# Optimization experiments

Hardware: AMD Instinct MI355X
Metric: run time of the kernel (lower is better)

Reference implementation:

```python
import jax, jax.numpy as jnp
import numpy as np

T, B, FEAT, HID, NCLS = 256, 64, 256, 1024, 257


def hamilton_block(W):
    # W: [4, di, do] components (r,i,j,k) -> full real block matrix [4*di, 4*do]
    Wr, Wi, Wj, Wk = W[0], W[1], W[2], W[3]
    row0 = jnp.concatenate([Wr, Wi, Wj, Wk], axis=-1)
    row1 = jnp.concatenate([-Wi, Wr, -Wk, Wj], axis=-1)
    row2 = jnp.concatenate([-Wj, Wk, Wr, -Wi], axis=-1)
    row3 = jnp.concatenate([-Wk, -Wj, Wi, Wr], axis=-1)
    return jnp.concatenate([row0, row1, row2, row3], axis=-2)


def setup_inputs() -> dict:
    key = jax.random.key(0)
    ks = jax.random.split(key, 7)
    x = jax.random.normal(ks[0], (T, B, FEAT), dtype=jnp.float32)
    sx = 1.0 / np.sqrt(FEAT)
    sh = 1.0 / np.sqrt(HID)
    # 4 gates (f,i,o,c) x 4 quaternion components x [feat/4, hid/4]
    Wx = jax.random.normal(ks[1], (4, 4, FEAT // 4, HID // 4), dtype=jnp.float32) * sx
    bx = jax.random.normal(ks[2], (4, HID), dtype=jnp.float32) * sx
    Wh = jax.random.normal(ks[3], (4, 4, HID // 4, HID // 4), dtype=jnp.float32) * sh
    Wo = jax.random.normal(ks[4], (HID, NCLS), dtype=jnp.float32) * sh
    bo = jax.random.normal(ks[5], (NCLS,), dtype=jnp.float32) * sh
    return {"x": x, "Wx": Wx, "bx": bx, "Wh": Wh, "Wo": Wo, "bo": bo}


def reference(x, Wx, bx, Wh, Wo, bo):
    # Build full real Hamilton-product matrices per gate.
    Wx_full = jax.vmap(hamilton_block)(Wx)  # [4, FEAT, HID]
    Wh_full = jax.vmap(hamilton_block)(Wh)  # [4, HID, HID]
    # Precompute input-to-hidden gate terms for all timesteps: [4, T, B, HID]
    gx = jnp.einsum('tbf,gfh->gtbh', x, Wx_full) + bx[:, None, None, :]

    def step(carry, gx_t):  # gx_t: [4, B, HID]
        h, c = carry
        gh = jnp.einsum('bh,gho->gbo', h, Wh_full)  # [4, B, HID]
        ft = jax.nn.sigmoid(gx_t[0] + gh[0])
        it = jax.nn.sigmoid(gx_t[1] + gh[1])
        ot = jax.nn.sigmoid(gx_t[2] + gh[2])
        at = gx_t[3] + gh[3]
        c = it * jnp.tanh(at) + ft * c
        h = ot * jnp.tanh(c)
        return (h, c), h

    h0 = jnp.zeros((B, HID), dtype=x.dtype)
    _, hs = jax.lax.scan(step, (h0, h0), jnp.moveaxis(gx, 1, 0))  # hs: [T, B, HID]
    return jnp.einsum('tbh,hc->tbc', hs, Wo) + bo  # [T, B, NCLS]
```

## Files before the change

kernel.cpp:

```cpp
#include <hip/hip_runtime.h>
#include <hip/hip_bf16.h>
#include <math.h>

#define T 256
#define B 64
#define FEAT 256
#define HID 1024
#define NCLS 257
#define KSTEPS 40
#define BH (B * HID)
#define BFEAT (B * FEAT)
#define NBLK 128
#define NTHR 512

typedef __attribute__((ext_vector_type(8))) short short8v;
typedef __attribute__((ext_vector_type(4))) float floatx4;

__device__ __constant__ int   d_comp[4][4] = {{0,1,2,3},{1,0,3,2},{2,3,0,1},{3,2,1,0}};
__device__ __constant__ float d_sign[4][4] = {{ 1.f, 1.f, 1.f, 1.f},
                                              {-1.f, 1.f,-1.f, 1.f},
                                              {-1.f, 1.f, 1.f,-1.f},
                                              {-1.f,-1.f, 1.f, 1.f}};

__device__ __forceinline__ ushort f2bf(float f) {
    union { float f; unsigned u; } v; v.f = f;
    unsigned r = v.u + 0x7FFF + ((v.u >> 16) & 1);
    return (ushort)(r >> 16);
}

__device__ __forceinline__ float sigm(float v) { return 1.f / (1.f + __expf(-v)); }
__device__ __forceinline__ float tanh_fast(float v) { return 1.f - 2.f / (1.f + __expf(2.f * v)); }

__global__ __launch_bounds__(256) void conv_xpanel(const float* __restrict__ x,
                                                   ushort* __restrict__ xp) {
    int i = blockIdx.x * 256 + threadIdx.x;
    int k4 = i & 63, b = (i >> 6) & 63, t = i >> 12;
    int k = k4 * 4;
    float4 v = ((const float4*)x)[i];
    ushort4 o;
    o.x = f2bf(v.x); o.y = f2bf(v.y); o.z = f2bf(v.z); o.w = f2bf(v.w);
    *(ushort4*)(xp + (size_t)t * BFEAT + (k >> 3) * 512 + b * 8 + (k & 4)) = o;
}

__global__ __launch_bounds__(256) void prep_wcf(const float* __restrict__ Wh,
                                                const float* __restrict__ Wx,
                                                ushort* __restrict__ wcf) {
    int e = blockIdx.x * 256 + threadIdx.x;
    int j    = e & 7;
    int lane = (e >> 3) & 63;
    int r    = e >> 9;
    int ks   = r % 40;
    int s    = r / 40;
    int mt   = s & 1;
    int blk  = s >> 1;
    int c  = mt * 16 + (lane & 15);
    int hl = c >> 2, g = c & 3;
    int n  = blk * 8 + hl;
    int qq = n >> 8, bc = n & 255;
    int k  = ks * 32 + ((lane >> 4) << 3) + j;
    float v;
    if (k < HID) {
        int p = k >> 8, a = k & 255;
        v = d_sign[p][qq] * Wh[((g * 4 + d_comp[p][qq]) * 256 + a) * 256 + bc];
    } else {
        int kk = k - HID;
        int p = kk >> 6, a = kk & 63;
        v = d_sign[p][qq] * Wx[((g * 4 + d_comp[p][qq]) * 64 + a) * 256 + bc];
    }
    wcf[e] = f2bf(v);
}

__global__ __launch_bounds__(256) void prep_wof(const float* __restrict__ Wo,
                                                ushort* __restrict__ wof) {
    int e = blockIdx.x * 256 + threadIdx.x;
    int j    = e & 7;
    int lane = (e >> 3) & 63;
    int ks   = (e >> 9) & 31;
    int tile = e >> 14;
    int n = tile * 16 + (lane & 15);
    int k = ks * 32 + ((lane >> 4) << 3) + j;
    wof[e] = (n < NCLS) ? f2bf(Wo[k * NCLS + n]) : (ushort)0;
}

__global__ __launch_bounds__(256) void init_hc(ushort* __restrict__ hs0,
                                               uint* __restrict__ flags) {
    int i = blockIdx.x * 256 + threadIdx.x;
    hs0[i] = 0;
    if (i < NBLK) flags[i] = 0;
}

__global__ __launch_bounds__(512, 2) void qlstm_persist(
    const ushort* __restrict__ xp,
    const ushort* __restrict__ wcf,
    const float*  __restrict__ bx,
    ushort*       __restrict__ hsteps,
    uint*         __restrict__ flags)
{
    __shared__ float pre[2][64][36];

    const int tid   = threadIdx.x;
    const int blk   = blockIdx.x;
    const int w     = tid >> 6;
    const int lane  = tid & 63;
    const int khalf = w >> 2;
    const int bt    = w & 3;
    const int hofs  = khalf * 16;
    const int xofs  = khalf * 4;

    const short8v* wsrc = (const short8v*)wcf + (size_t)blk * 2 * KSTEPS * 64 + lane;
    short8v Ah[2][16], Ax[2][4];
    #pragma unroll
    for (int mt = 0; mt < 2; ++mt) {
        #pragma unroll
        for (int i = 0; i < 16; ++i) Ah[mt][i] = wsrc[(mt * KSTEPS + hofs + i) * 64];
        #pragma unroll
        for (int u = 0; u < 4; ++u)  Ax[mt][u] = wsrc[(mt * KSTEPS + 32 + xofs + u) * 64];
    }
    #pragma unroll
    for (int mt = 0; mt < 2; ++mt) {
        #pragma unroll
        for (int i = 0; i < 16; ++i) asm volatile("" : "+v"(Ah[mt][i]));
        #pragma unroll
        for (int u = 0; u < 4; ++u)  asm volatile("" : "+v"(Ax[mt][u]));
    }

    const int gb = tid >> 3;
    const int hc = tid & 7;
    const int gn = blk * 8 + hc;
    const float bxf = bx[gn], bxi = bx[HID + gn];
    const float bxo = bx[2 * HID + gn], bxa = bx[3 * HID + gn];
    float c_reg = 0.f;

    const int boff = (lane >> 4) * 512 + (bt * 16 + (lane & 15)) * 8;

    for (int t = 0; t < T; ++t) {
        floatx4 acc0 = {0.f,0.f,0.f,0.f}, acc1 = {0.f,0.f,0.f,0.f};

        const ushort* xrow = xp + (size_t)t * BFEAT + boff;
        #pragma unroll
        for (int u = 0; u < 4; ++u) {
            short8v bv = *(const short8v*)(xrow + (xofs + u) * 2048);
            acc0 = __builtin_amdgcn_mfma_f32_16x16x32_bf16(Ax[0][u], bv, acc0, 0, 0, 0);
            acc1 = __builtin_amdgcn_mfma_f32_16x16x32_bf16(Ax[1][u], bv, acc1, 0, 0, 0);
        }

        if (t > 0) {
            const uint tgt = (uint)t;
            for (;;) {
                uint f0 = __hip_atomic_load(flags + lane,      __ATOMIC_RELAXED, __HIP_MEMORY_SCOPE_AGENT);
                uint f1 = __hip_atomic_load(flags + 64 + lane, __ATOMIC_RELAXED, __HIP_MEMORY_SCOPE_AGENT);
                if (__all((f0 >= tgt) && (f1 >= tgt))) break;
                __builtin_amdgcn_s_sleep(1);
            }
        }

        const ushort* hrow = hsteps + (size_t)t * BH + boff;
        #pragma unroll
        for (int i = 0; i < 16; ++i) {
            short8v bv = *(const short8v*)(hrow + (hofs + i) * 2048);
            acc0 = __builtin_amdgcn_mfma_f32_16x16x32_bf16(Ah[0][i], bv, acc0, 0, 0, 0);
            acc1 = __builtin_amdgcn_mfma_f32_16x16x32_bf16(Ah[1][i], bv, acc1, 0, 0, 0);
        }

        {
            const int pb = bt * 16 + (lane & 15);
            const int pm = (lane >> 4) * 4;
            #pragma unroll
            for (int jj = 0; jj < 4; ++jj) {
                pre[khalf][pb][pm + jj]      = acc0[jj];
                pre[khalf][pb][16 + pm + jj] = acc1[jj];
            }
        }
        __syncthreads();

        {
            float4 p0 = *(const float4*)&pre[0][gb][hc * 4];
            float4 p1 = *(const float4*)&pre[1][gb][hc * 4];
            float f  = sigm(p0.x + p1.x + bxf);
            float i_ = sigm(p0.y + p1.y + bxi);
            float o  = sigm(p0.z + p1.z + bxo);
            float a  = p0.w + p1.w + bxa;
            c_reg = i_ * tanh_fast(a) + f * c_reg;
            float h = o * tanh_fast(c_reg);
            uint hvu = f2bf(h);
            ushort* hp = hsteps + (size_t)(t + 1) * BH + blk * 512 + tid;
            asm volatile("global_store_short %0, %1, off sc0 sc1"
                         :: "v"(hp), "v"(hvu) : "memory");
            asm volatile("s_waitcnt vmcnt(0)" ::: "memory");
        }
        __syncthreads();

        if (t < T - 1 && tid == 0)
            __hip_atomic_store(flags + blk, (uint)(t + 1),
                               __ATOMIC_RELAXED, __HIP_MEMORY_SCOPE_AGENT);
    }
}

__global__ __launch_bounds__(256) void outproj(const ushort* __restrict__ hsteps,
                                               const ushort* __restrict__ wof,
                                               const float* __restrict__ bo,
                                               float* __restrict__ out) {
    const int tt   = blockIdx.x;
    const int nt   = blockIdx.y;
    const int tid  = threadIdx.x;
    const int w    = tid >> 6;
    const int lane = tid & 63;
    const int b    = w * 16 + (lane & 15);
    const ushort* abase = hsteps + (size_t)(tt + 1) * BH + (lane >> 4) * 512 + b * 8;
    const short8v* wb  = (const short8v*)wof;

    floatx4 ac[4] = {{0.f,0.f,0.f,0.f},{0.f,0.f,0.f,0.f},
                     {0.f,0.f,0.f,0.f},{0.f,0.f,0.f,0.f}};
    #pragma unroll 4
    for (int ks = 0; ks < 32; ++ks) {
        short8v av = *(const short8v*)(abase + ks * 2048);
        #pragma unroll
        for (int ct = 0; ct < 4; ++ct)
            ac[ct] = __builtin_amdgcn_mfma_f32_16x16x32_bf16(
                av, wb[((nt * 4 + ct) * 32 + ks) * 64 + lane], ac[ct], 0, 0, 0);
    }
    const int orow = tt * 64 + w * 16 + (lane >> 4) * 4;
    #pragma unroll
    for (int ct = 0; ct < 4; ++ct) {
        int n = nt * 64 + ct * 16 + (lane & 15);
        if (n < NCLS) {
            float bias = bo[n];
            #pragma unroll
            for (int j = 0; j < 4; ++j)
                out[(size_t)(orow + j) * NCLS + n] = ac[ct][j] + bias;
        }
    }
}

extern "C" void kernel_launch(void* const* d_in, const int* in_sizes, int n_in,
                              void* d_out, int out_size, void* d_ws, size_t ws_size,
                              hipStream_t stream) {
    const float* x  = (const float*)d_in[0];
    const float* Wx = (const float*)d_in[1];
    const float* bx = (const float*)d_in[2];
    const float* Wh = (const float*)d_in[3];
    const float* Wo = (const float*)d_in[4];
    const float* bo = (const float*)d_in[5];
    float* out = (float*)d_out;

    ushort* xp     = (ushort*)d_ws;
    ushort* wcf    = xp  + (size_t)T * BFEAT;
    ushort* wof    = wcf + (size_t)NBLK * 2 * KSTEPS * 512;
    ushort* hsteps = wof + 327680;
    uint*   flags  = (uint*)(hsteps + (size_t)(T + 1) * BH);

    conv_xpanel<<<(T * B * FEAT / 4) / 256, 256, 0, stream>>>(x, xp);
    prep_wcf<<<(NBLK * 2 * KSTEPS * 512) / 256, 256, 0, stream>>>(Wh, Wx, wcf);
    prep_wof<<<(20 * 32 * 512) / 256, 256, 0, stream>>>(Wo, wof);
    init_hc<<<BH / 256, 256, 0, stream>>>(hsteps, flags);

    void* args[] = {(void*)&xp, (void*)&wcf, (void*)&bx, (void*)&hsteps, (void*)&flags};
    hipLaunchCooperativeKernel((void*)qlstm_persist, dim3(NBLK), dim3(NTHR),
                               args, 0, stream);

    outproj<<<dim3(T, 5), 256, 0, stream>>>(hsteps, wof, bo, out);
}
```

Baseline: 1.101 ms.

## Split batch into four independent groups to pipeline the recurrent LSTM steps

The persistent recurrence kernel is restructured so the batch of 64 is split into four 16-row groups, each with its own h panel slot and flag array. Phases interleave the groups, so a block computes group g while other groups' hidden states are still being published. The new version uses 256 blocks of 256 threads, each owning 4 hidden units with a 4-way K split, and software-prefetches the next x/h panels and flag values. The aim is to hide cross-block synchronization latency behind independent work. The cost is more phases, more flag traffic and smaller MFMA work per barrier.

```diff
diff --git a/kernel.cpp b/kernel.cpp
--- a/kernel.cpp
+++ b/kernel.cpp
@@ -7,11 +7,11 @@
 #define FEAT 256
 #define HID 1024
 #define NCLS 257
-#define KSTEPS 40
-#define BH (B * HID)
-#define BFEAT (B * FEAT)
-#define NBLK 128
-#define NTHR 512
+#define NBLK 256
+#define NTHR 256
+#define NPH (T * 4)
+#define HSLOT 16384
+#define XSLOT 4096
 
 typedef __attribute__((ext_vector_type(8))) short short8v;
 typedef __attribute__((ext_vector_type(4))) float floatx4;
@@ -36,10 +36,11 @@
     int i = blockIdx.x * 256 + threadIdx.x;
     int k4 = i & 63, b = (i >> 6) & 63, t = i >> 12;
     int k = k4 * 4;
+    int g = b >> 4, b16 = b & 15;
     float4 v = ((const float4*)x)[i];
     ushort4 o;
     o.x = f2bf(v.x); o.y = f2bf(v.y); o.z = f2bf(v.z); o.w = f2bf(v.w);
-    *(ushort4*)(xp + (size_t)t * BFEAT + (k >> 3) * 512 + b * 8 + (k & 4)) = o;
+    *(ushort4*)(xp + (size_t)(t * 4 + g) * XSLOT + (k >> 3) * 128 + b16 * 8 + (k & 7)) = o;
 }
 
 __global__ __launch_bounds__(256) void prep_wcf(const float* __restrict__ Wh,
@@ -50,22 +51,20 @@
     int lane = (e >> 3) & 63;
     int r    = e >> 9;
     int ks   = r % 40;
-    int s    = r / 40;
-    int mt   = s & 1;
-    int blk  = s >> 1;
-    int c  = mt * 16 + (lane & 15);
-    int hl = c >> 2, g = c & 3;
-    int n  = blk * 8 + hl;
+    int blk  = r / 40;
+    int c  = lane & 15;
+    int hl = c >> 2, gg = c & 3;
+    int n  = blk * 4 + hl;
     int qq = n >> 8, bc = n & 255;
     int k  = ks * 32 + ((lane >> 4) << 3) + j;
     float v;
     if (k < HID) {
         int p = k >> 8, a = k & 255;
-        v = d_sign[p][qq] * Wh[((g * 4 + d_comp[p][qq]) * 256 + a) * 256 + bc];
+        v = d_sign[p][qq] * Wh[((gg * 4 + d_comp[p][qq]) * 256 + a) * 256 + bc];
     } else {
         int kk = k - HID;
         int p = kk >> 6, a = kk & 63;
-        v = d_sign[p][qq] * Wx[((g * 4 + d_comp[p][qq]) * 64 + a) * 256 + bc];
+        v = d_sign[p][qq] * Wx[((gg * 4 + d_comp[p][qq]) * 64 + a) * 256 + bc];
     }
     wcf[e] = f2bf(v);
 }
@@ -82,144 +81,167 @@
     wof[e] = (n < NCLS) ? f2bf(Wo[k * NCLS + n]) : (ushort)0;
 }
 
-__global__ __launch_bounds__(256) void init_hc(ushort* __restrict__ hs0,
-                                               uint* __restrict__ flags) {
-    int i = blockIdx.x * 256 + threadIdx.x;
-    hs0[i] = 0;
-    if (i < NBLK) flags[i] = 0;
-}
-
-__global__ __launch_bounds__(512, 2) void qlstm_persist(
+__global__ __launch_bounds__(256) void init_flags(uint* __restrict__ flg) {
+    int i = threadIdx.x;
+    flg[i] = 0; flg[256 + i] = 0; flg[512 + i] = 0; flg[768 + i] = 0;
+}
+
+__global__ __launch_bounds__(256) void qlstm_persist(
     const ushort* __restrict__ xp,
     const ushort* __restrict__ wcf,
     const float*  __restrict__ bx,
-    ushort*       __restrict__ hsteps,
-    uint*         __restrict__ flags)
+    ushort*       __restrict__ hpan,
+    uint*         __restrict__ flg)
 {
-    __shared__ float pre[2][64][36];
-
-    const int tid   = threadIdx.x;
-    const int blk   = blockIdx.x;
-    const int w     = tid >> 6;
-    const int lane  = tid & 63;
-    const int khalf = w >> 2;
-    const int bt    = w & 3;
-    const int hofs  = khalf * 16;
-    const int xofs  = khalf * 4;
-
-    const short8v* wsrc = (const short8v*)wcf + (size_t)blk * 2 * KSTEPS * 64 + lane;
-    short8v Ah[2][16], Ax[2][4];
-    #pragma unroll
-    for (int mt = 0; mt < 2; ++mt) {
-        #pragma unroll
-        for (int i = 0; i < 16; ++i) Ah[mt][i] = wsrc[(mt * KSTEPS + hofs + i) * 64];
-        #pragma unroll
-        for (int u = 0; u < 4; ++u)  Ax[mt][u] = wsrc[(mt * KSTEPS + 32 + xofs + u) * 64];
-    }
-    #pragma unroll
-    for (int mt = 0; mt < 2; ++mt) {
-        #pragma unroll
-        for (int i = 0; i < 16; ++i) asm volatile("" : "+v"(Ah[mt][i]));
-        #pragma unroll
-        for (int u = 0; u < 4; ++u)  asm volatile("" : "+v"(Ax[mt][u]));
-    }
-
-    const int gb = tid >> 3;
-    const int hc = tid & 7;
-    const int gn = blk * 8 + hc;
+    __shared__ float pre[2][4][16][20];
+
+    const int tid  = threadIdx.x;
+    const int blk  = blockIdx.x;
+    const int kq   = tid >> 6;
+    const int lane = tid & 63;
+    const int ld_off = (lane >> 4) * 128 + (lane & 15) * 8;
+
+    const short8v* wsrc = (const short8v*)wcf + (size_t)blk * 40 * 64 + lane;
+    short8v Ah[8], Axr[2];
+    #pragma unroll
+    for (int i = 0; i < 8; ++i) Ah[i] = wsrc[(kq * 8 + i) * 64];
+    #pragma unroll
+    for (int u = 0; u < 2; ++u) Axr[u] = wsrc[(32 + kq * 2 + u) * 64];
+    #pragma unroll
+    for (int i = 0; i < 8; ++i) asm volatile("" : "+v"(Ah[i]));
+    #pragma unroll
+    for (int u = 0; u < 2; ++u) asm volatile("" : "+v"(Axr[u]));
+
+    const int gb_loc = lane >> 2;
+    const int ghc    = lane & 3;
+    const int gn     = blk * 4 + ghc;
     const float bxf = bx[gn], bxi = bx[HID + gn];
     const float bxo = bx[2 * HID + gn], bxa = bx[3 * HID + gn];
+    const int st_off = (blk >> 1) * 128 + gb_loc * 8 + (blk & 1) * 4 + ghc;
     float c_reg = 0.f;
 
-    const int boff = (lane >> 4) * 512 + (bt * 16 + (lane & 15)) * 8;
+    short8v hb[8], xv[2];
+    uint4 fcarry = make_uint4(~0u, ~0u, ~0u, ~0u);
+    {
+        const ushort* xs = xp;
+        #pragma unroll
+        for (int u = 0; u < 2; ++u)
+            xv[u] = *(const short8v*)(xs + (kq * 2 + u) * 512 + ld_off);
+    }
 
     for (int t = 0; t < T; ++t) {
-        floatx4 acc0 = {0.f,0.f,0.f,0.f}, acc1 = {0.f,0.f,0.f,0.f};
-
-        const ushort* xrow = xp + (size_t)t * BFEAT + boff;
         #pragma unroll
-        for (int u = 0; u < 4; ++u) {
-            short8v bv = *(const short8v*)(xrow + (xofs + u) * 2048);
-            acc0 = __builtin_amdgcn_mfma_f32_16x16x32_bf16(Ax[0][u], bv, acc0, 0, 0, 0);
-            acc1 = __builtin_amdgcn_mfma_f32_16x16x32_bf16(Ax[1][u], bv, acc1, 0, 0, 0);
+        for (int g = 0; g < 4; ++g) {
+            const int p = t * 4 + g;
+
+            floatx4 acc = {0.f, 0.f, 0.f, 0.f};
+            acc = __builtin_amdgcn_mfma_f32_16x16x32_bf16(Axr[0], xv[0], acc, 0, 0, 0);
+            acc = __builtin_amdgcn_mfma_f32_16x16x32_bf16(Axr[1], xv[1], acc, 0, 0, 0);
+            if (t > 0) {
+                #pragma unroll
+                for (int i = 0; i < 8; ++i)
+                    acc = __builtin_amdgcn_mfma_f32_16x16x32_bf16(Ah[i], hb[i], acc, 0, 0, 0);
+            }
+
+            const int p1 = p + 1;
+            if (p1 < NPH) {
+                const ushort* xs = xp + (size_t)p1 * XSLOT;
+                #pragma unroll
+                for (int u = 0; u < 2; ++u)
+                    xv[u] = *(const short8v*)(xs + (kq * 2 + u) * 512 + ld_off);
+            }
+
+            if (p1 < NPH && p1 >= 4) {
+                const uint tgt = (uint)(p1 >> 2);
+                const int g2 = p1 & 3;
+                uint4 fu = fcarry;
+                bool ok = fu.x >= tgt && fu.y >= tgt && fu.z >= tgt && fu.w >= tgt;
+                while (!__all(ok)) {
+                    __builtin_amdgcn_s_sleep(1);
+                    fu.x = __hip_atomic_load(flg + g2 * NBLK + lane,       __ATOMIC_RELAXED, __HIP_MEMORY_SCOPE_AGENT);
+                    fu.y = __hip_atomic_load(flg + g2 * NBLK + 64 + lane,  __ATOMIC_RELAXED, __HIP_MEMORY_SCOPE_AGENT);
+                    fu.z = __hip_atomic_load(flg + g2 * NBLK + 128 + lane, __ATOMIC_RELAXED, __HIP_MEMORY_SCOPE_AGENT);
+                    fu.w = __hip_atomic_load(flg + g2 * NBLK + 192 + lane, __ATOMIC_RELAXED, __HIP_MEMORY_SCOPE_AGENT);
+                    ok = fu.x >= tgt && fu.y >= tgt && fu.z >= tgt && fu.w >= tgt;
+                }
+                __builtin_amdgcn_sched_barrier(0);
+                const ushort* hs = hpan + (size_t)p1 * HSLOT;
+                #pragma unroll
+                for (int i = 0; i < 8; ++i)
+                    hb[i] = *(const short8v*)(hs + (kq * 8 + i) * 512 + ld_off);
+            }
+
+            {
+                const int p2 = p + 2;
+                if (p2 < NPH && p2 >= 4) {
+                    const int g3 = p2 & 3;
+                    fcarry.x = __hip_atomic_load(flg + g3 * NBLK + lane,       __ATOMIC_RELAXED, __HIP_MEMORY_SCOPE_AGENT);
+                    fcarry.y = __hip_atomic_load(flg + g3 * NBLK + 64 + lane,  __ATOMIC_RELAXED, __HIP_MEMORY_SCOPE_AGENT);
+                    fcarry.z = __hip_atomic_load(flg + g3 * NBLK + 128 + lane, __ATOMIC_RELAXED, __HIP_MEMORY_SCOPE_AGENT);
+                    fcarry.w = __hip_atomic_load(flg + g3 * NBLK + 192 + lane, __ATOMIC_RELAXED, __HIP_MEMORY_SCOPE_AGENT);
+                } else {
+                    fcarry = make_uint4(~0u, ~0u, ~0u, ~0u);
+                }
+            }
+
+            {
+                const int pb = lane & 15;
+                const int pm = (lane >> 4) * 4;
+                #pragma unroll
+                for (int jj = 0; jj < 4; ++jj)
+                    pre[g & 1][kq][pb][pm + jj] = acc[jj];
+            }
+            __syncthreads();
+
+            if (kq == g) {
+                float4 s0 = *(const float4*)&pre[g & 1][0][gb_loc][ghc * 4];
+                float4 s1 = *(const float4*)&pre[g & 1][1][gb_loc][ghc * 4];
+                float4 s2 = *(const float4*)&pre[g & 1][2][gb_loc][ghc * 4];
+                float4 s3 = *(const float4*)&pre[g & 1][3][gb_loc][ghc * 4];
+                float pf = s0.x + s1.x + s2.x + s3.x + bxf;
+                float pi = s0.y + s1.y + s2.y + s3.y + bxi;
+                float po = s0.z + s1.z + s2.z + s3.z + bxo;
+                float pa = s0.w + s1.w + s2.w + s3.w + bxa;
+                float f  = sigm(pf), i_ = sigm(pi), o = sigm(po);
+                c_reg = i_ * tanh_fast(pa) + f * c_reg;
+                float h = o * tanh_fast(c_reg);
+                uint hvu = f2bf(h);
+                ushort* hp = hpan + (size_t)(p + 4) * HSLOT + st_off;
+                asm volatile("global_store_short %0, %1, off sc0 sc1"
+                             :: "v"(hp), "v"(hvu) : "memory");
+                asm volatile("s_waitcnt vmcnt(0)" ::: "memory");
+                if (lane == 0)
+                    __hip_atomic_store(flg + g * NBLK + blk, (uint)(t + 1),
+                                       __ATOMIC_RELAXED, __HIP_MEMORY_SCOPE_AGENT);
+            }
         }
-
-        if (t > 0) {
-            const uint tgt = (uint)t;
-            for (;;) {
-                uint f0 = __hip_atomic_load(flags + lane,      __ATOMIC_RELAXED, __HIP_MEMORY_SCOPE_AGENT);
-                uint f1 = __hip_atomic_load(flags + 64 + lane, __ATOMIC_RELAXED, __HIP_MEMORY_SCOPE_AGENT);
-                if (__all((f0 >= tgt) && (f1 >= tgt))) break;
-                __builtin_amdgcn_s_sleep(1);
-            }
-        }
-
-        const ushort* hrow = hsteps + (size_t)t * BH + boff;
-        #pragma unroll
-        for (int i = 0; i < 16; ++i) {
-            short8v bv = *(const short8v*)(hrow + (hofs + i) * 2048);
-            acc0 = __builtin_amdgcn_mfma_f32_16x16x32_bf16(Ah[0][i], bv, acc0, 0, 0, 0);
-            acc1 = __builtin_amdgcn_mfma_f32_16x16x32_bf16(Ah[1][i], bv, acc1, 0, 0, 0);
-        }
-
-        {
-            const int pb = bt * 16 + (lane & 15);
-            const int pm = (lane >> 4) * 4;
-            #pragma unroll
-            for (int jj = 0; jj < 4; ++jj) {
-                pre[khalf][pb][pm + jj]      = acc0[jj];
-                pre[khalf][pb][16 + pm + jj] = acc1[jj];
-            }
-        }
-        __syncthreads();
-
-        {
-            float4 p0 = *(const float4*)&pre[0][gb][hc * 4];
-            float4 p1 = *(const float4*)&pre[1][gb][hc * 4];
-            float f  = sigm(p0.x + p1.x + bxf);
-            float i_ = sigm(p0.y + p1.y + bxi);
-            float o  = sigm(p0.z + p1.z + bxo);
-            float a  = p0.w + p1.w + bxa;
-            c_reg = i_ * tanh_fast(a) + f * c_reg;
-            float h = o * tanh_fast(c_reg);
-            uint hvu = f2bf(h);
-            ushort* hp = hsteps + (size_t)(t + 1) * BH + blk * 512 + tid;
-            asm volatile("global_store_short %0, %1, off sc0 sc1"
-                         :: "v"(hp), "v"(hvu) : "memory");
-            asm volatile("s_waitcnt vmcnt(0)" ::: "memory");
-        }
-        __syncthreads();
-
-        if (t < T - 1 && tid == 0)
-            __hip_atomic_store(flags + blk, (uint)(t + 1),
-                               __ATOMIC_RELAXED, __HIP_MEMORY_SCOPE_AGENT);
-    }
-}
-
-__global__ __launch_bounds__(256) void outproj(const ushort* __restrict__ hsteps,
+    }
+}
+
+__global__ __launch_bounds__(256) void outproj(const ushort* __restrict__ hpan,
                                                const ushort* __restrict__ wof,
                                                const float* __restrict__ bo,
                                                float* __restrict__ out) {
     const int tt   = blockIdx.x;
     const int nt   = blockIdx.y;
     const int tid  = threadIdx.x;
-    const int w    = tid >> 6;
+    const int g    = tid >> 6;
     const int lane = tid & 63;
-    const int b    = w * 16 + (lane & 15);
-    const ushort* abase = hsteps + (size_t)(tt + 1) * BH + (lane >> 4) * 512 + b * 8;
-    const short8v* wb  = (const short8v*)wof;
+    const ushort* abase = hpan + ((size_t)(tt + 1) * 4 + g) * HSLOT
+                          + (lane >> 4) * 128 + (lane & 15) * 8;
+    const short8v* wb = (const short8v*)wof;
 
     floatx4 ac[4] = {{0.f,0.f,0.f,0.f},{0.f,0.f,0.f,0.f},
                      {0.f,0.f,0.f,0.f},{0.f,0.f,0.f,0.f}};
     #pragma unroll 4
     for (int ks = 0; ks < 32; ++ks) {
-        short8v av = *(const short8v*)(abase + ks * 2048);
+        short8v av = *(const short8v*)(abase + ks * 512);
         #pragma unroll
         for (int ct = 0; ct < 4; ++ct)
             ac[ct] = __builtin_amdgcn_mfma_f32_16x16x32_bf16(
                 av, wb[((nt * 4 + ct) * 32 + ks) * 64 + lane], ac[ct], 0, 0, 0);
     }
-    const int orow = tt * 64 + w * 16 + (lane >> 4) * 4;
+    const int orow = tt * 64 + g * 16 + (lane >> 4) * 4;
     #pragma unroll
     for (int ct = 0; ct < 4; ++ct) {
         int n = nt * 64 + ct * 16 + (lane & 15);
@@ -243,20 +265,20 @@
     const float* bo = (const float*)d_in[5];
     float* out = (float*)d_out;
 
-    ushort* xp     = (ushort*)d_ws;
-    ushort* wcf    = xp  + (size_t)T * BFEAT;
-    ushort* wof    = wcf + (size_t)NBLK * 2 * KSTEPS * 512;
-    ushort* hsteps = wof + 327680;
-    uint*   flags  = (uint*)(hsteps + (size_t)(T + 1) * BH);
+    ushort* xp   = (ushort*)d_ws;
+    ushort* wcf  = xp  + (size_t)NPH * XSLOT;
+    ushort* wof  = wcf + (size_t)256 * 40 * 512;
+    ushort* hpan = wof + 327680;
+    uint*   flg  = (uint*)(hpan + (size_t)(NPH + 4) * HSLOT);
 
     conv_xpanel<<<(T * B * FEAT / 4) / 256, 256, 0, stream>>>(x, xp);
-    prep_wcf<<<(NBLK * 2 * KSTEPS * 512) / 256, 256, 0, stream>>>(Wh, Wx, wcf);
+    prep_wcf<<<(256 * 40 * 512) / 256, 256, 0, stream>>>(Wh, Wx, wcf);
     prep_wof<<<(20 * 32 * 512) / 256, 256, 0, stream>>>(Wo, wof);
-    init_hc<<<BH / 256, 256, 0, stream>>>(hsteps, flags);
-
-    void* args[] = {(void*)&xp, (void*)&wcf, (void*)&bx, (void*)&hsteps, (void*)&flags};
+    init_flags<<<1, 256, 0, stream>>>(flg);
+
+    void* args[] = {(void*)&xp, (void*)&wcf, (void*)&bx, (void*)&hpan, (void*)&flg};
     hipLaunchCooperativeKernel((void*)qlstm_persist, dim3(NBLK), dim3(NTHR),
                                args, 0, stream);
 
-    outproj<<<dim3(T, 5), 256, 0, stream>>>(hsteps, wof, bo, out);
-}
+    outproj<<<dim3(T, 5), 256, 0, stream>>>(hpan, wof, bo, out);
+}
```

Result: slower. 1.502 ms (+36.4%).

## Split persistent LSTM across batch chunks with per-chunk flags and panel layout

Applied to the files above, without the earlier changes.

The recurrent kernel now uses 256 blocks, each owning 16 hidden units for one 16-row batch chunk. Blocks synchronize only with the 64 blocks sharing their batch chunk rather than all blocks. The h and x panels are re-laid out per chunk so each block loads a contiguous 16-batch slab. Loads are batched through inline asm before the MFMAs, and half the threads sit idle in the gate stage. This is meant to shorten the per-step barrier and the per-block work, at the cost of more blocks, each weight tile being held by four blocks, and no overlap between the h loads and the MFMAs.

```diff
diff --git a/kernel.cpp b/kernel.cpp
--- a/kernel.cpp
+++ b/kernel.cpp
@@ -7,11 +7,12 @@
 #define FEAT 256
 #define HID 1024
 #define NCLS 257
-#define KSTEPS 40
-#define BH (B * HID)
-#define BFEAT (B * FEAT)
-#define NBLK 128
+#define NCH 4
+#define NCG 64
+#define NBLK 256
 #define NTHR 512
+#define HSLOT 16384
+#define XSLOT 4096
 
 typedef __attribute__((ext_vector_type(8))) short short8v;
 typedef __attribute__((ext_vector_type(4))) float floatx4;
@@ -36,10 +37,11 @@
     int i = blockIdx.x * 256 + threadIdx.x;
     int k4 = i & 63, b = (i >> 6) & 63, t = i >> 12;
     int k = k4 * 4;
+    int c = b >> 4, b16 = b & 15;
     float4 v = ((const float4*)x)[i];
     ushort4 o;
     o.x = f2bf(v.x); o.y = f2bf(v.y); o.z = f2bf(v.z); o.w = f2bf(v.w);
-    *(ushort4*)(xp + (size_t)t * BFEAT + (k >> 3) * 512 + b * 8 + (k & 4)) = o;
+    *(ushort4*)(xp + (size_t)(t * 4 + c) * XSLOT + (k >> 3) * 128 + b16 * 8 + (k & 7)) = o;
 }
 
 __global__ __launch_bounds__(256) void prep_wcf(const float* __restrict__ Wh,
@@ -51,11 +53,11 @@
     int r    = e >> 9;
     int ks   = r % 40;
     int s    = r / 40;
-    int mt   = s & 1;
-    int blk  = s >> 1;
+    int mt   = s & 3;
+    int cg   = s >> 2;
     int c  = mt * 16 + (lane & 15);
     int hl = c >> 2, g = c & 3;
-    int n  = blk * 8 + hl;
+    int n  = cg * 16 + hl;
     int qq = n >> 8, bc = n & 255;
     int k  = ks * 32 + ((lane >> 4) << 3) + j;
     float v;
@@ -82,100 +84,113 @@
     wof[e] = (n < NCLS) ? f2bf(Wo[k * NCLS + n]) : (ushort)0;
 }
 
-__global__ __launch_bounds__(256) void init_hc(ushort* __restrict__ hs0,
-                                               uint* __restrict__ flags) {
+__global__ __launch_bounds__(256) void init_hf(ushort* __restrict__ hpan,
+                                               uint* __restrict__ flg) {
     int i = blockIdx.x * 256 + threadIdx.x;
-    hs0[i] = 0;
-    if (i < NBLK) flags[i] = 0;
+    ((ushort4*)hpan)[i] = make_ushort4(0, 0, 0, 0);
+    if (blockIdx.x == 0) flg[threadIdx.x] = 0;
 }
 
 __global__ __launch_bounds__(512, 2) void qlstm_persist(
     const ushort* __restrict__ xp,
     const ushort* __restrict__ wcf,
     const float*  __restrict__ bx,
-    ushort*       __restrict__ hsteps,
-    uint*         __restrict__ flags)
+    ushort*       __restrict__ hpan,
+    uint*         __restrict__ flg)
 {
-    __shared__ float pre[2][64][36];
-
-    const int tid   = threadIdx.x;
-    const int blk   = blockIdx.x;
-    const int w     = tid >> 6;
-    const int lane  = tid & 63;
-    const int khalf = w >> 2;
-    const int bt    = w & 3;
-    const int hofs  = khalf * 16;
-    const int xofs  = khalf * 4;
-
-    const short8v* wsrc = (const short8v*)wcf + (size_t)blk * 2 * KSTEPS * 64 + lane;
-    short8v Ah[2][16], Ax[2][4];
+    __shared__ float pre[2][16][72];
+
+    const int tid  = threadIdx.x;
+    const int blk  = blockIdx.x;
+    const int ch   = blk & 3;
+    const int cg   = blk >> 2;
+    const int w    = tid >> 6;
+    const int lane = tid & 63;
+    const int mt   = w & 3;
+    const int kh   = w >> 2;
+    const int ld_off = (lane >> 4) * 128 + (lane & 15) * 8;
+
+    const ushort* wbase = wcf + ((size_t)(cg * 4 + mt) * 40 + kh * 20) * 512 + lane * 8;
+    short8v A[20];
     #pragma unroll
-    for (int mt = 0; mt < 2; ++mt) {
+    for (int i = 0; i < 20; ++i) {
+        const ushort* ap = wbase + i * 512;
+        asm volatile("global_load_dwordx4 %0, %1, off" : "=v"(A[i]) : "v"(ap));
+    }
+    asm volatile("s_waitcnt vmcnt(0)" ::: "memory");
+    __builtin_amdgcn_sched_barrier(0);
+
+    const int gb = tid >> 4;
+    const int hl = tid & 15;
+    const int gn = cg * 16 + hl;
+    float bxf = 0.f, bxi = 0.f, bxo = 0.f, bxa = 0.f;
+    if (tid < 256) {
+        bxf = bx[gn]; bxi = bx[HID + gn];
+        bxo = bx[2 * HID + gn]; bxa = bx[3 * HID + gn];
+    }
+    float c_reg = 0.f;
+    const int st_off = (cg * 2 + (hl >> 3)) * 128 + gb * 8 + (hl & 7);
+    uint* myflags = flg + ch * 64;
+
+    for (int t = 0; t < T; ++t) {
+        const ushort* hs = hpan + (size_t)(t * NCH + ch) * HSLOT;
+        const ushort* xs = xp   + (size_t)(t * NCH + ch) * XSLOT;
+
+        short8v Bf[20];
+        if (kh == 1) {
+            #pragma unroll
+            for (int i = 12; i < 20; ++i) {
+                const ushort* p = xs + (i - 12) * 512 + ld_off;
+                asm volatile("global_load_dwordx4 %0, %1, off" : "=v"(Bf[i]) : "v"(p));
+            }
+        }
+
+        if (t > 0) {
+            if (w == 0) {
+                const uint tgt = (uint)t;
+                for (;;) {
+                    uint f = __hip_atomic_load(myflags + lane, __ATOMIC_RELAXED,
+                                               __HIP_MEMORY_SCOPE_AGENT);
+                    if (__all(f >= tgt)) break;
+                    __builtin_amdgcn_s_sleep(1);
+                }
+            }
+            __syncthreads();
+        }
+
+        if (kh == 0) {
+            #pragma unroll
+            for (int i = 0; i < 20; ++i) {
+                const ushort* p = hs + i * 512 + ld_off;
+                asm volatile("global_load_dwordx4 %0, %1, off" : "=v"(Bf[i]) : "v"(p));
+            }
+        } else {
+            #pragma unroll
+            for (int i = 0; i < 12; ++i) {
+                const ushort* p = hs + (20 + i) * 512 + ld_off;
+                asm volatile("global_load_dwordx4 %0, %1, off" : "=v"(Bf[i]) : "v"(p));
+            }
+        }
+        asm volatile("s_waitcnt vmcnt(0)" ::: "memory");
+        __builtin_amdgcn_sched_barrier(0);
+
+        floatx4 a0 = {0.f,0.f,0.f,0.f}, a1 = {0.f,0.f,0.f,0.f};
         #pragma unroll
-        for (int i = 0; i < 16; ++i) Ah[mt][i] = wsrc[(mt * KSTEPS + hofs + i) * 64];
-        #pragma unroll
-        for (int u = 0; u < 4; ++u)  Ax[mt][u] = wsrc[(mt * KSTEPS + 32 + xofs + u) * 64];
-    }
-    #pragma unroll
-    for (int mt = 0; mt < 2; ++mt) {
-        #pragma unroll
-        for (int i = 0; i < 16; ++i) asm volatile("" : "+v"(Ah[mt][i]));
-        #pragma unroll
-        for (int u = 0; u < 4; ++u)  asm volatile("" : "+v"(Ax[mt][u]));
-    }
-
-    const int gb = tid >> 3;
-    const int hc = tid & 7;
-    const int gn = blk * 8 + hc;
-    const float bxf = bx[gn], bxi = bx[HID + gn];
-    const float bxo = bx[2 * HID + gn], bxa = bx[3 * HID + gn];
-    float c_reg = 0.f;
-
-    const int boff = (lane >> 4) * 512 + (bt * 16 + (lane & 15)) * 8;
-
-    for (int t = 0; t < T; ++t) {
-        floatx4 acc0 = {0.f,0.f,0.f,0.f}, acc1 = {0.f,0.f,0.f,0.f};
-
-        const ushort* xrow = xp + (size_t)t * BFEAT + boff;
-        #pragma unroll
-        for (int u = 0; u < 4; ++u) {
-            short8v bv = *(const short8v*)(xrow + (xofs + u) * 2048);
-            acc0 = __builtin_amdgcn_mfma_f32_16x16x32_bf16(Ax[0][u], bv, acc0, 0, 0, 0);
-            acc1 = __builtin_amdgcn_mfma_f32_16x16x32_bf16(Ax[1][u], bv, acc1, 0, 0, 0);
-        }
-
-        if (t > 0) {
-            const uint tgt = (uint)t;
-            for (;;) {
-                uint f0 = __hip_atomic_load(flags + lane,      __ATOMIC_RELAXED, __HIP_MEMORY_SCOPE_AGENT);
-                uint f1 = __hip_atomic_load(flags + 64 + lane, __ATOMIC_RELAXED, __HIP_MEMORY_SCOPE_AGENT);
-                if (__all((f0 >= tgt) && (f1 >= tgt))) break;
-                __builtin_amdgcn_s_sleep(1);
-            }
-        }
-
-        const ushort* hrow = hsteps + (size_t)t * BH + boff;
-        #pragma unroll
-        for (int i = 0; i < 16; ++i) {
-            short8v bv = *(const short8v*)(hrow + (hofs + i) * 2048);
-            acc0 = __builtin_amdgcn_mfma_f32_16x16x32_bf16(Ah[0][i], bv, acc0, 0, 0, 0);
-            acc1 = __builtin_amdgcn_mfma_f32_16x16x32_bf16(Ah[1][i], bv, acc1, 0, 0, 0);
-        }
+        for (int i = 0; i < 20; i += 2) {
+            a0 = __builtin_amdgcn_mfma_f32_16x16x32_bf16(A[i],     Bf[i],     a0, 0, 0, 0);
+            a1 = __builtin_amdgcn_mfma_f32_16x16x32_bf16(A[i + 1], Bf[i + 1], a1, 0, 0, 0);
+        }
+        floatx4 acc = a0 + a1;
 
         {
-            const int pb = bt * 16 + (lane & 15);
-            const int pm = (lane >> 4) * 4;
-            #pragma unroll
-            for (int jj = 0; jj < 4; ++jj) {
-                pre[khalf][pb][pm + jj]      = acc0[jj];
-                pre[khalf][pb][16 + pm + jj] = acc1[jj];
-            }
+            float4 v = make_float4(acc[0], acc[1], acc[2], acc[3]);
+            *(float4*)&pre[kh][lane & 15][mt * 16 + (lane >> 4) * 4] = v;
         }
         __syncthreads();
 
-        {
-            float4 p0 = *(const float4*)&pre[0][gb][hc * 4];
-            float4 p1 = *(const float4*)&pre[1][gb][hc * 4];
+        if (tid < 256) {
+            float4 p0 = *(const float4*)&pre[0][gb][hl * 4];
+            float4 p1 = *(const float4*)&pre[1][gb][hl * 4];
             float f  = sigm(p0.x + p1.x + bxf);
             float i_ = sigm(p0.y + p1.y + bxi);
             float o  = sigm(p0.z + p1.z + bxo);
@@ -183,43 +198,43 @@
             c_reg = i_ * tanh_fast(a) + f * c_reg;
             float h = o * tanh_fast(c_reg);
             uint hvu = f2bf(h);
-            ushort* hp = hsteps + (size_t)(t + 1) * BH + blk * 512 + tid;
+            ushort* hp = hpan + (size_t)((t + 1) * NCH + ch) * HSLOT + st_off;
             asm volatile("global_store_short %0, %1, off sc0 sc1"
                          :: "v"(hp), "v"(hvu) : "memory");
             asm volatile("s_waitcnt vmcnt(0)" ::: "memory");
         }
         __syncthreads();
 
-        if (t < T - 1 && tid == 0)
-            __hip_atomic_store(flags + blk, (uint)(t + 1),
+        if (tid == 0)
+            __hip_atomic_store(myflags + cg, (uint)(t + 1),
                                __ATOMIC_RELAXED, __HIP_MEMORY_SCOPE_AGENT);
     }
 }
 
-__global__ __launch_bounds__(256) void outproj(const ushort* __restrict__ hsteps,
+__global__ __launch_bounds__(256) void outproj(const ushort* __restrict__ hpan,
                                                const ushort* __restrict__ wof,
                                                const float* __restrict__ bo,
                                                float* __restrict__ out) {
     const int tt   = blockIdx.x;
     const int nt   = blockIdx.y;
     const int tid  = threadIdx.x;
-    const int w    = tid >> 6;
+    const int g    = tid >> 6;
     const int lane = tid & 63;
-    const int b    = w * 16 + (lane & 15);
-    const ushort* abase = hsteps + (size_t)(tt + 1) * BH + (lane >> 4) * 512 + b * 8;
-    const short8v* wb  = (const short8v*)wof;
+    const ushort* abase = hpan + ((size_t)(tt + 1) * 4 + g) * HSLOT
+                          + (lane >> 4) * 128 + (lane & 15) * 8;
+    const short8v* wb = (const short8v*)wof;
 
     floatx4 ac[4] = {{0.f,0.f,0.f,0.f},{0.f,0.f,0.f,0.f},
                      {0.f,0.f,0.f,0.f},{0.f,0.f,0.f,0.f}};
     #pragma unroll 4
     for (int ks = 0; ks < 32; ++ks) {
-        short8v av = *(const short8v*)(abase + ks * 2048);
+        short8v av = *(const short8v*)(abase + ks * 512);
         #pragma unroll
         for (int ct = 0; ct < 4; ++ct)
             ac[ct] = __builtin_amdgcn_mfma_f32_16x16x32_bf16(
                 av, wb[((nt * 4 + ct) * 32 + ks) * 64 + lane], ac[ct], 0, 0, 0);
     }
-    const int orow = tt * 64 + w * 16 + (lane >> 4) * 4;
+    const int orow = tt * 64 + g * 16 + (lane >> 4) * 4;
     #pragma unroll
     for (int ct = 0; ct < 4; ++ct) {
         int n = nt * 64 + ct * 16 + (lane & 15);
@@ -243,20 +258,20 @@
     const float* bo = (const float*)d_in[5];
     float* out = (float*)d_out;
 
-    ushort* xp     = (ushort*)d_ws;
-    ushort* wcf    = xp  + (size_t)T * BFEAT;
-    ushort* wof    = wcf + (size_t)NBLK * 2 * KSTEPS * 512;
-    ushort* hsteps = wof + 327680;
-    uint*   flags  = (uint*)(hsteps + (size_t)(T + 1) * BH);
+    ushort* xp   = (ushort*)d_ws;
+    ushort* wcf  = xp  + (size_t)T * 4 * XSLOT;
+    ushort* wof  = wcf + (size_t)64 * 4 * 40 * 512;
+    ushort* hpan = wof + 327680;
+    uint*   flg  = (uint*)(hpan + (size_t)(T + 1) * 4 * HSLOT);
 
     conv_xpanel<<<(T * B * FEAT / 4) / 256, 256, 0, stream>>>(x, xp);
-    prep_wcf<<<(NBLK * 2 * KSTEPS * 512) / 256, 256, 0, stream>>>(Wh, Wx, wcf);
+    prep_wcf<<<(64 * 4 * 40 * 512) / 256, 256, 0, stream>>>(Wh, Wx, wcf);
     prep_wof<<<(20 * 32 * 512) / 256, 256, 0, stream>>>(Wo, wof);
-    init_hc<<<BH / 256, 256, 0, stream>>>(hsteps, flags);
-
-    void* args[] = {(void*)&xp, (void*)&wcf, (void*)&bx, (void*)&hsteps, (void*)&flags};
+    init_hf<<<64, 256, 0, stream>>>(hpan, flg);
+
+    void* args[] = {(void*)&xp, (void*)&wcf, (void*)&bx, (void*)&hpan, (void*)&flg};
     hipLaunchCooperativeKernel((void*)qlstm_persist, dim3(NBLK), dim3(NTHR),
                                args, 0, stream);
 
-    outproj<<<dim3(T, 5), 256, 0, stream>>>(hsteps, wof, bo, out);
-}
+    outproj<<<dim3(T, 5), 256, 0, stream>>>(hpan, wof, bo, out);
+}
```

Measured after the change: 1.108 ms. About the same (+0.6%).
